# Kernel tuning notes

Hardware: AMD Instinct MI355X
Metric: run time of the kernel (lower is better)

Reference implementation:

```python
import jax, jax.numpy as jnp
import numpy as np

B, S, DIM, H, HD = 4, 1024, 1280, 16, 80
SCALE = HD ** -0.5
ROPE_THETA = 10000.0


def rotate_half(x):
    x1, x2 = jnp.split(x, 2, axis=-1)
    return jnp.concatenate([-x2, x1], axis=-1)


def setup_inputs() -> dict:
    key = jax.random.key(0)
    ks = jax.random.split(key, 5)
    x = jax.random.normal(ks[0], (B, S, DIM), dtype=jnp.float32)
    Wqkv = jax.random.normal(ks[1], (DIM, 3 * DIM), dtype=jnp.float32) * 0.02
    bqkv = jax.random.normal(ks[2], (3 * DIM,), dtype=jnp.float32) * 0.01
    Wproj = jax.random.normal(ks[3], (DIM, DIM), dtype=jnp.float32) * 0.02
    bproj = jax.random.normal(ks[4], (DIM,), dtype=jnp.float32) * 0.01
    # realistic rotary tables: (S, HD) with duplicated freq halves (matches rotate_half layout)
    inv_freq = 1.0 / (ROPE_THETA ** (jnp.arange(0, HD, 2, dtype=jnp.float32) / HD))
    freqs = jnp.outer(jnp.arange(S, dtype=jnp.float32), inv_freq)  # (S, HD/2)
    emb = jnp.concatenate([freqs, freqs], axis=-1)  # (S, HD)
    rope_cos = jnp.cos(emb)
    rope_sin = jnp.sin(emb)
    return {"x": x, "rope_cos": rope_cos, "rope_sin": rope_sin,
            "Wqkv": Wqkv, "bqkv": bqkv, "Wproj": Wproj, "bproj": bproj}


def reference(x, rope_cos, rope_sin, Wqkv, bqkv, Wproj, bproj):
    b, s, d = x.shape
    qkv = (x @ Wqkv + bqkv).reshape(b, s, 3, H, HD)
    q, k, v = qkv[:, :, 0], qkv[:, :, 1], qkv[:, :, 2]  # each (b, s, H, HD)
    cos = rope_cos[None, :, None, :]  # (1, s, 1, HD)
    sin = rope_sin[None, :, None, :]
    q = q * cos + rotate_half(q) * sin
    k = k * cos + rotate_half(k) * sin
    # SDPA with all-ones mask (full attention)
    scores = jnp.einsum("bqhd,bkhd->bhqk", q, k) * SCALE
    probs = jax.nn.softmax(scores, axis=-1)
    out = jnp.einsum("bhqk,bkhd->bqhd", probs, v).reshape(b, s, d)
    return out @ Wproj + bproj
```

## Files before the change

### kernel.cpp

```cpp
#include <hip/hip_runtime.h>
#include <math.h>

#define SCALE_F 0.11180339887498949f
#define HDP 96

typedef short  short8  __attribute__((ext_vector_type(8)));
typedef short  short4v __attribute__((ext_vector_type(4)));
typedef float  f32x4   __attribute__((ext_vector_type(4)));
typedef __bf16 bf16x8  __attribute__((ext_vector_type(8)));

__device__ __forceinline__ float bf2f(short s) {
  union { unsigned u; float f; } v;
  v.u = ((unsigned)(unsigned short)s) << 16;
  return v.f;
}
__device__ __forceinline__ short f2b(float f) {
  __bf16 h = (__bf16)f;
  return __builtin_bit_cast(short, h);
}
__device__ __forceinline__ bool probe_is_bf16(const unsigned* probe) {
  return (probe[1] & 0xFFFFu) != 0u;
}
__device__ __forceinline__ float load_scalar(const void* p, int i, bool isb) {
  return isb ? bf2f(((const short*)p)[i]) : ((const float*)p)[i];
}

__device__ __forceinline__ void gload_lds16(const short* g, short* l) {
  __builtin_amdgcn_global_load_lds(
      (const __attribute__((address_space(1))) void*)g,
      (__attribute__((address_space(3))) void*)l, 16, 0, 0);
}

template <typename V>
__device__ __forceinline__ auto mfma_try(V a, V b, f32x4 c, int)
    -> decltype(__builtin_amdgcn_mfma_f32_16x16x32_bf16(a, b, c, 0, 0, 0)) {
  return __builtin_amdgcn_mfma_f32_16x16x32_bf16(a, b, c, 0, 0, 0);
}
template <typename V>
__device__ __forceinline__ f32x4 mfma_try(V a, V b, f32x4 c, long) {
  return __builtin_amdgcn_mfma_f32_16x16x32_bf16(
      __builtin_bit_cast(bf16x8, a), __builtin_bit_cast(bf16x8, b), c, 0, 0, 0);
}
__device__ __forceinline__ f32x4 MFMA(short8 a, short8 b, f32x4 c) {
  return mfma_try(a, b, c, 0);
}

__global__ __launch_bounds__(256) void cvt_x_kernel(
    const void* __restrict__ xin, short* __restrict__ xout,
    const unsigned* __restrict__ probe) {
  bool isb = probe_is_bf16(probe);
  size_t i = ((size_t)blockIdx.x * 256 + threadIdx.x) * 8;
  if (isb) {
    *(short8*)&xout[i] = *(const short8*)((const short*)xin + i);
  } else {
    const float* f = (const float*)xin + i;
    float4 a0 = *(const float4*)f;
    float4 a1 = *(const float4*)(f + 4);
    short8 sv;
    sv[0] = f2b(a0.x); sv[1] = f2b(a0.y); sv[2] = f2b(a0.z); sv[3] = f2b(a0.w);
    sv[4] = f2b(a1.x); sv[5] = f2b(a1.y); sv[6] = f2b(a1.z); sv[7] = f2b(a1.w);
    *(short8*)&xout[i] = sv;
  }
}

__global__ __launch_bounds__(256) void transpose_kernel(
    const void* __restrict__ in, short* __restrict__ out, int R, int C,
    const unsigned* __restrict__ probe) {
  bool isb = probe_is_bf16(probe);
  __shared__ float tile[32][33];
  int t = threadIdx.x;
  int bx = blockIdx.x;
  int by = blockIdx.y;
  int r = t >> 3, c4 = (t & 7) * 4;
  size_t idx = (size_t)(by * 32 + r) * C + bx * 32 + c4;
  if (isb) {
    short4v v = *(const short4v*)((const short*)in + idx);
    tile[r][c4 + 0] = bf2f(v[0]);
    tile[r][c4 + 1] = bf2f(v[1]);
    tile[r][c4 + 2] = bf2f(v[2]);
    tile[r][c4 + 3] = bf2f(v[3]);
  } else {
    float4 v = *(const float4*)((const float*)in + idx);
    tile[r][c4 + 0] = v.x;
    tile[r][c4 + 1] = v.y;
    tile[r][c4 + 2] = v.z;
    tile[r][c4 + 3] = v.w;
  }
  __syncthreads();
  int rr = t >> 3, k4 = (t & 7) * 4;
  short4v o;
  o[0] = f2b(tile[k4 + 0][rr]);
  o[1] = f2b(tile[k4 + 1][rr]);
  o[2] = f2b(tile[k4 + 2][rr]);
  o[3] = f2b(tile[k4 + 3][rr]);
  *(short4v*)&out[(size_t)(bx * 32 + rr) * R + by * 32 + k4] = o;
}

__global__ __launch_bounds__(512, 2) void gemm_qkv_kernel(
    const short* __restrict__ X, const short* __restrict__ Wt,
    const void* __restrict__ bias, const unsigned* __restrict__ probe,
    short* __restrict__ Qw, short* __restrict__ Kw, short* __restrict__ Vt) {
  const int K = 1280;
  __shared__ short Al[2][2][8192];
  __shared__ short Bl[2][2][8192];
  int t = threadIdx.x;
  int bm = blockIdx.x / 15, bn = blockIdx.x % 15;
  int m0 = bm * 256, n0 = bn * 256;
  int w = t >> 6, lane = t & 63;
  int quad = lane >> 4, l16 = lane & 15, l8 = l16 & 7;
  int arow = (w >> 2) * 64 + l16;
  int brow = (w & 3) * 32 + l16;
  int sr = t >> 3, t8s = t * 8;
  int sjs = (t & 7) ^ (sr & 7);
  int soff0 = ((quad ^ l8) * 8);
  int soff1 = (((4 + quad) ^ l8) * 8);
  f32x4 acc[2][2][4][2] = {};
  short8 afr[4][2];
  short8 bf0[2][2], bf1[2][2];

#define STAGE8(PTR, R0, KOFF, LP)                                            \
  {                                                                          \
    const short* g_ = (PTR) + (size_t)((R0) + sr) * 1280 + (KOFF) + sjs * 8; \
    gload_lds16(g_, (LP) + t8s);                                             \
    gload_lds16(g_ + 64 * 1280, (LP) + t8s + 4096);                          \
  }

#define READ_A(S, H)                                                         \
  {                                                                          \
    _Pragma("unroll") for (int mt = 0; mt < 4; mt++) {                       \
      int rp_ = (arow + mt * 16) * 64;                                       \
      afr[mt][0] = *(const short8*)&Al[S][H][rp_ + soff0];                   \
      afr[mt][1] = *(const short8*)&Al[S][H][rp_ + soff1];                   \
    }                                                                        \
  }
#define READ_B(DST, S, H)                                                    \
  {                                                                          \
    _Pragma("unroll") for (int nt = 0; nt < 2; nt++) {                       \
      int rp_ = (brow + nt * 16) * 64;                                       \
      DST[nt][0] = *(const short8*)&Bl[S][H][rp_ + soff0];                   \
      DST[nt][1] = *(const short8*)&Bl[S][H][rp_ + soff1];                   \
    }                                                                        \
  }
#define MFMA16(QM, QN, BF, WAITI)                                            \
  {                                                                          \
    asm volatile("s_waitcnt lgkmcnt(" #WAITI ")" ::: "memory");              \
    __builtin_amdgcn_sched_barrier(0);                                       \
    __builtin_amdgcn_s_setprio(1);                                           \
    _Pragma("unroll") for (int mt = 0; mt < 4; mt++)                         \
      _Pragma("unroll") for (int nt = 0; nt < 2; nt++) {                     \
        acc[QM][QN][mt][nt] = MFMA(afr[mt][0], BF[nt][0], acc[QM][QN][mt][nt]); \
        acc[QM][QN][mt][nt] = MFMA(afr[mt][1], BF[nt][1], acc[QM][QN][mt][nt]); \
      }                                                                      \
    __builtin_amdgcn_s_setprio(0);                                           \
  }
#define BAR() __builtin_amdgcn_s_barrier()
#define VW4()                                                                \
  {                                                                          \
    asm volatile("s_waitcnt vmcnt(4)" ::: "memory");                         \
    __builtin_amdgcn_sched_barrier(0);                                       \
  }

  STAGE8(X,  m0,       0,  &Al[0][0][0]);
  STAGE8(X,  m0 + 128, 0,  &Al[0][1][0]);
  STAGE8(Wt, n0,       0,  &Bl[0][0][0]);
  STAGE8(Wt, n0 + 128, 0,  &Bl[0][1][0]);
  STAGE8(X,  m0,       64, &Al[1][0][0]);
  STAGE8(Wt, n0,       64, &Bl[1][0][0]);
  VW4();
  BAR();

  for (int i = 0; i < 10; i++) {
    int k1 = (2 * i + 1) * 64;
    int k2 = (2 * i + 2) * 64; if (k2 >= K) k2 = 0;
    int k3 = (2 * i + 3) * 64; if (k3 >= K) k3 = 0;
    READ_A(0, 0); READ_B(bf0, 0, 0); READ_B(bf1, 0, 1);
    STAGE8(X,  m0 + 128, k1, &Al[1][1][0]);
    MFMA16(0, 0, bf0, 4);
    BAR();
    STAGE8(Wt, n0 + 128, k1, &Bl[1][1][0]);
    MFMA16(0, 1, bf1, 0);
    BAR();
    READ_A(0, 1);
    STAGE8(X,  m0,       k2, &Al[0][0][0]);
    MFMA16(1, 0, bf0, 0);
    BAR();
    STAGE8(Wt, n0,       k2, &Bl[0][0][0]);
    MFMA16(1, 1, bf1, 0);
    VW4();
    BAR();
    READ_A(1, 0); READ_B(bf0, 1, 0); READ_B(bf1, 1, 1);
    STAGE8(X,  m0 + 128, k2, &Al[0][1][0]);
    MFMA16(0, 0, bf0, 4);
    BAR();
    STAGE8(Wt, n0 + 128, k2, &Bl[0][1][0]);
    MFMA16(0, 1, bf1, 0);
    BAR();
    READ_A(1, 1);
    STAGE8(X,  m0,       k3, &Al[1][0][0]);
    MFMA16(1, 0, bf0, 0);
    BAR();
    STAGE8(Wt, n0,       k3, &Bl[1][0][0]);
    MFMA16(1, 1, bf1, 0);
    VW4();
    BAR();
  }
  asm volatile("s_waitcnt vmcnt(0)" ::: "memory");
  __builtin_amdgcn_sched_barrier(0);

  bool isb = probe_is_bf16(probe);
  float bv[2][2];
#pragma unroll
  for (int qn = 0; qn < 2; qn++)
#pragma unroll
    for (int nt = 0; nt < 2; nt++)
      bv[qn][nt] =
          load_scalar(bias, n0 + qn * 128 + (w & 3) * 32 + nt * 16 + l16, isb);
#pragma unroll
  for (int qm = 0; qm < 2; qm++)
#pragma unroll
    for (int mt = 0; mt < 4; mt++) {
      int mbase = m0 + qm * 128 + (w >> 2) * 64 + mt * 16 + quad * 4;
      int b = mbase >> 10, sbase = mbase & 1023;
#pragma unroll
      for (int qn = 0; qn < 2; qn++)
#pragma unroll
        for (int nt = 0; nt < 2; nt++) {
          int n = n0 + qn * 128 + (w & 3) * 32 + nt * 16 + l16;
          int which = n / 1280;
          int rmod = n - which * 1280;
          int h = rmod / 80;
          int d = rmod - h * 80;
          int bh = b * 16 + h;
          if (which == 2) {
            short4v vv;
#pragma unroll
            for (int reg = 0; reg < 4; reg++)
              vv[reg] = f2b(acc[qm][qn][mt][nt][reg] + bv[qn][nt]);
            *(short4v*)&Vt[((size_t)bh * 80 + d) * 1024 + sbase] = vv;
          } else {
            short* dst = (which == 0 ? Qw : Kw);
#pragma unroll
            for (int reg = 0; reg < 4; reg++)
              dst[((size_t)bh * 1024 + sbase + reg) * HDP + d] =
                  f2b(acc[qm][qn][mt][nt][reg] + bv[qn][nt]);
          }
        }
    }
#undef STAGE8
#undef READ_A
#undef READ_B
#undef MFMA16
#undef BAR
#undef VW4
}

__global__ __launch_bounds__(256) void rope_kernel(
    short* __restrict__ Qw, short* __restrict__ Kw,
    const void* __restrict__ cosb, const void* __restrict__ sinb,
    const unsigned* __restrict__ probe) {
  bool isb = probe_is_bf16(probe);
  int t = threadIdx.x;
  int w = t >> 6, lane = t & 63;
  int job = blockIdx.x * 4 + w;
  int which = job & 1;
  int row = job >> 1;
  int s = row & 1023;
  short* ptr = (which ? Kw : Qw) + (size_t)row * HDP;
  float scale = which ? 1.0f : SCALE_F;
  if (lane < 40) {
    float p0 = bf2f(ptr[lane]);
    float p1 = bf2f(ptr[lane + 40]);
    float c0 = load_scalar(cosb, s * 80 + lane, isb);
    float s0 = load_scalar(sinb, s * 80 + lane, isb);
    float c1 = load_scalar(cosb, s * 80 + lane + 40, isb);
    float s1 = load_scalar(sinb, s * 80 + lane + 40, isb);
    ptr[lane] = f2b((p0 * c0 - p1 * s0) * scale);
    ptr[lane + 40] = f2b((p1 * c1 + p0 * s1) * scale);
  } else if (lane < 56) {
    ptr[40 + lane] = 0;
  }
}

__global__ __launch_bounds__(512, 4) void attn_kernel(
    const short* __restrict__ Qw, const short* __restrict__ Kw,
    const short* __restrict__ Vt, short* __restrict__ out) {
  __shared__ short Klds[2][64 * 104];
  __shared__ short Vlds[2][80 * 72];
  __shared__ short Ps[8][16 * 72];
  int t = threadIdx.x;
  int w = t >> 6, lane = t & 63;
  int quad = lane >> 4, l16 = lane & 15;
  int bh = blockIdx.x & 63;
  int qt = blockIdx.x >> 6;
  int q0 = qt * 128;
  const short* Kb = Kw + (size_t)bh * 1024 * HDP;
  const short* Vb = Vt + (size_t)bh * 80 * 1024;

  short8 aq[3];
  {
    const short* qrow = Qw + ((size_t)bh * 1024 + q0 + w * 16 + l16) * HDP;
#pragma unroll
    for (int ks = 0; ks < 3; ks++)
      aq[ks] = *(const short8*)&qrow[ks * 32 + quad * 8];
  }

  short8 kreg[2], vreg[2];
#define PREFETCH(c)                                                        \
  {                                                                        \
    {                                                                      \
      int row = t / 12, col = (t % 12) * 8;                                \
      kreg[0] = *(const short8*)&Kb[(size_t)((c) + row) * HDP + col];      \
    }                                                                      \
    if (t < 256) {                                                         \
      int idx = 512 + t;                                                   \
      int row = idx / 12, col = (idx % 12) * 8;                            \
      kreg[1] = *(const short8*)&Kb[(size_t)((c) + row) * HDP + col];      \
    }                                                                      \
    {                                                                      \
      int d = t >> 3, s0 = (t & 7) * 8;                                    \
      vreg[0] = *(const short8*)&Vb[(size_t)d * 1024 + (c) + s0];          \
    }                                                                      \
    if (t < 128) {                                                         \
      int idx = 512 + t;                                                   \
      int d = idx >> 3, s0 = (idx & 7) * 8;                                \
      vreg[1] = *(const short8*)&Vb[(size_t)d * 1024 + (c) + s0];          \
    }                                                                      \
  }
#define STORE_LDS(P)                                                       \
  {                                                                        \
    {                                                                      \
      int row = t / 12, col = (t % 12) * 8;                                \
      *(short8*)&Klds[P][row * 104 + col] = kreg[0];                       \
    }                                                                      \
    if (t < 256) {                                                         \
      int idx = 512 + t;                                                   \
      int row = idx / 12, col = (idx % 12) * 8;                            \
      *(short8*)&Klds[P][row * 104 + col] = kreg[1];                       \
    }                                                                      \
    {                                                                      \
      int d = t >> 3, s0 = (t & 7) * 8;                                    \
      *(short8*)&Vlds[P][d * 72 + s0] = vreg[0];                           \
    }                                                                      \
    if (t < 128) {                                                         \
      int idx = 512 + t;                                                   \
      int d = idx >> 3, s0 = (idx & 7) * 8;                                \
      *(short8*)&Vlds[P][d * 72 + s0] = vreg[1];                           \
    }                                                                      \
  }

  PREFETCH(0);
  STORE_LDS(0);
  __syncthreads();

  f32x4 ofr[5] = {};
  float lsum[4] = {0.f, 0.f, 0.f, 0.f};
  short* Pw = &Ps[w][0];

  int p = 0;
  for (int c = 0; c < 1024; c += 64, p ^= 1) {
    if (c + 64 < 1024) PREFETCH(c + 64);
    const short* Kl = &Klds[p][0];
    const short* Vl = &Vlds[p][0];
    f32x4 sf[4] = {};
#pragma unroll
    for (int nt = 0; nt < 4; nt++) {
      short8 bk0 = *(const short8*)&Kl[(nt * 16 + l16) * 104 + 0 * 32 + quad * 8];
      short8 bk1 = *(const short8*)&Kl[(nt * 16 + l16) * 104 + 1 * 32 + quad * 8];
      short8 bk2 = *(const short8*)&Kl[(nt * 16 + l16) * 104 + 2 * 32 + quad * 8];
      sf[nt] = MFMA(aq[0], bk0, sf[nt]);
      sf[nt] = MFMA(aq[1], bk1, sf[nt]);
      sf[nt] = MFMA(aq[2], bk2, sf[nt]);
    }
#pragma unroll
    for (int r = 0; r < 4; r++) {
      float p0 = __expf(fminf(sf[0][r], 30.f));
      float p1 = __expf(fminf(sf[1][r], 30.f));
      float p2 = __expf(fminf(sf[2][r], 30.f));
      float p3 = __expf(fminf(sf[3][r], 30.f));
      sf[0][r] = p0; sf[1][r] = p1; sf[2][r] = p2; sf[3][r] = p3;
      lsum[r] += (p0 + p1) + (p2 + p3);
    }
#pragma unroll
    for (int nt = 0; nt < 4; nt++)
#pragma unroll
      for (int r = 0; r < 4; r++)
        Pw[(quad * 4 + r) * 72 + nt * 16 + l16] = f2b(sf[nt][r]);
    __threadfence_block();
    short8 ap[2];
#pragma unroll
    for (int ks = 0; ks < 2; ks++)
      ap[ks] = *(const short8*)&Pw[l16 * 72 + ks * 32 + quad * 8];
#pragma unroll
    for (int nt = 0; nt < 5; nt++) {
      short8 bv0 = *(const short8*)&Vl[(nt * 16 + l16) * 72 + 0 * 32 + quad * 8];
      short8 bv1 = *(const short8*)&Vl[(nt * 16 + l16) * 72 + 1 * 32 + quad * 8];
      ofr[nt] = MFMA(ap[0], bv0, ofr[nt]);
      ofr[nt] = MFMA(ap[1], bv1, ofr[nt]);
    }
    if (c + 64 < 1024) {
      STORE_LDS(p ^ 1);
      __syncthreads();
    }
  }
#pragma unroll
  for (int off = 1; off < 16; off <<= 1)
#pragma unroll
    for (int r = 0; r < 4; r++) lsum[r] += __shfl_xor(lsum[r], off);
  float inv[4];
#pragma unroll
  for (int r = 0; r < 4; r++) inv[r] = 1.f / lsum[r];
  int b = bh >> 4, h = bh & 15;
#pragma unroll
  for (int nt = 0; nt < 5; nt++) {
    int d = nt * 16 + l16;
#pragma unroll
    for (int r = 0; r < 4; r++) {
      int s = q0 + w * 16 + quad * 4 + r;
      out[((size_t)(b * 1024 + s)) * 1280 + h * 80 + d] = f2b(ofr[nt][r] * inv[r]);
    }
  }
}

__global__ __launch_bounds__(256) void gemm_proj_kernel(
    const short* __restrict__ A, const short* __restrict__ Wt,
    const void* __restrict__ bias, const unsigned* __restrict__ probe,
    float* __restrict__ out) {
  const int K = 1280;
  __shared__ short As[2][128 * 32];
  __shared__ short Bs[2][128 * 32];
  int t = threadIdx.x;
  int bm = blockIdx.x / 10;
  int bn = blockIdx.x % 10;
  int m0 = bm * 128, n0 = bn * 128;
  int w = t >> 6, lane = t & 63;
  int wm = w & 1, wn = w >> 1;
  int quad = lane >> 4, l16 = lane & 15;
  int row = t >> 2, ch = (t & 3) * 8, row2 = row + 64;
  int t8 = t * 8;
  const short* Ar  = A  + (size_t)(m0 + row)  * K + ch;
  const short* Ar2 = A  + (size_t)(m0 + row2) * K + ch;
  const short* Wr  = Wt + (size_t)(n0 + row)  * K + ch;
  const short* Wr2 = Wt + (size_t)(n0 + row2) * K + ch;
  f32x4 acc[4][4] = {};
  gload_lds16(Ar,  &As[0][t8]);
  gload_lds16(Ar2, &As[0][t8 + 2048]);
  gload_lds16(Wr,  &Bs[0][t8]);
  gload_lds16(Wr2, &Bs[0][t8 + 2048]);
  __syncthreads();
  int p = 0;
#define PROJ_COMPUTE(pp)                                                      \
  {                                                                           \
    short8 af[4], bfr[4];                                                     \
    _Pragma("unroll") for (int mt = 0; mt < 4; mt++)                          \
        af[mt] = *(const short8*)&As[pp][(wm * 64 + mt * 16 + l16) * 32 + quad * 8]; \
    _Pragma("unroll") for (int nt = 0; nt < 4; nt++)                          \
        bfr[nt] = *(const short8*)&Bs[pp][(wn * 64 + nt * 16 + l16) * 32 + quad * 8]; \
    _Pragma("unroll") for (int mt = 0; mt < 4; mt++)                          \
        _Pragma("unroll") for (int nt = 0; nt < 4; nt++)                      \
            acc[mt][nt] = MFMA(af[mt], bfr[nt], acc[mt][nt]);                 \
  }
  for (int k0 = 32; k0 < K; k0 += 32, p ^= 1) {
    gload_lds16(Ar + k0,  &As[p ^ 1][t8]);
    gload_lds16(Ar2 + k0, &As[p ^ 1][t8 + 2048]);
    gload_lds16(Wr + k0,  &Bs[p ^ 1][t8]);
    gload_lds16(Wr2 + k0, &Bs[p ^ 1][t8 + 2048]);
    PROJ_COMPUTE(p);
    __syncthreads();
  }
  PROJ_COMPUTE(p);
  bool isb = probe_is_bf16(probe);
  float bv[4];
#pragma unroll
  for (int nt = 0; nt < 4; nt++)
    bv[nt] = load_scalar(bias, n0 + wn * 64 + nt * 16 + l16, isb);
#pragma unroll
  for (int mt = 0; mt < 4; mt++) {
#pragma unroll
    for (int nt = 0; nt < 4; nt++) {
      int n = n0 + wn * 64 + nt * 16 + l16;
#pragma unroll
      for (int reg = 0; reg < 4; reg++) {
        int m = m0 + wm * 64 + mt * 16 + quad * 4 + reg;
        out[(size_t)m * 1280 + n] = acc[mt][nt][reg] + bv[nt];
      }
    }
  }
}

extern "C" void kernel_launch(void* const* d_in, const int* in_sizes, int n_in,
                              void* d_out, int out_size, void* d_ws, size_t ws_size,
                              hipStream_t stream) {
  const void* x        = d_in[0];
  const void* rope_cos = d_in[1];
  const void* rope_sin = d_in[2];
  const void* Wqkv     = d_in[3];
  const void* bqkv     = d_in[4];
  const void* Wproj    = d_in[5];
  const void* bproj    = d_in[6];
  const unsigned* probe = (const unsigned*)rope_cos;
  char* ws = (char*)d_ws;
  short* Wt1 = (short*)(ws + 0);
  short* Wt2 = (short*)(ws + 9830400);
  short* Qw  = (short*)(ws + 13107200);
  short* Kw  = (short*)(ws + 25690112);
  short* Vt  = (short*)(ws + 38273024);
  short* Xb  = (short*)(ws + 48758784);
  short* At  = (short*)(ws + 48758784);

  cvt_x_kernel<<<2560, 256, 0, stream>>>(x, Xb, probe);
  transpose_kernel<<<dim3(3840 / 32, 1280 / 32), 256, 0, stream>>>(Wqkv, Wt1, 1280, 3840, probe);
  transpose_kernel<<<dim3(1280 / 32, 1280 / 32), 256, 0, stream>>>(Wproj, Wt2, 1280, 1280, probe);
  gemm_qkv_kernel<<<240, 512, 0, stream>>>(Xb, Wt1, bqkv, probe, Qw, Kw, Vt);
  rope_kernel<<<32768, 256, 0, stream>>>(Qw, Kw, rope_cos, rope_sin, probe);
  attn_kernel<<<512, 512, 0, stream>>>(Qw, Kw, Vt, At);
  gemm_proj_kernel<<<32 * 10, 256, 0, stream>>>(At, Wt2, bproj, probe, (float*)d_out);
}
```

Measured before the change: 244.2 us.

## Keep attention probabilities in registers by computing transposed scores

Swaps the QK^T MFMA operands so each lane holds scores for one query row, letting the exponentiated probabilities feed directly as the B operand of 16x16x16 bf16 MFMAs for the PV product. This removes the per-wave LDS staging buffer for P, its write/read round trip, and the fence, and it simplifies the row-sum reduction and the output stores into vectorized short4 writes. The trade-off is twice as many smaller-K MFMA instructions for PV and 8-byte V reads from LDS.

New measurement: 236.9 us. -3.0%, faster.

```diff
diff --git a/kernel.cpp b/kernel.cpp
--- a/kernel.cpp
+++ b/kernel.cpp
@@ -8,6 +8,7 @@
 typedef short  short4v __attribute__((ext_vector_type(4)));
 typedef float  f32x4   __attribute__((ext_vector_type(4)));
 typedef __bf16 bf16x8  __attribute__((ext_vector_type(8)));
+typedef __bf16 bf16x4  __attribute__((ext_vector_type(4)));
 
 __device__ __forceinline__ float bf2f(short s) {
   union { unsigned u; float f; } v;
@@ -44,6 +45,42 @@
 __device__ __forceinline__ f32x4 MFMA(short8 a, short8 b, f32x4 c) {
   return mfma_try(a, b, c, 0);
 }
+
+#if __has_builtin(__builtin_amdgcn_mfma_f32_16x16x16bf16_1k)
+template <typename V>
+__device__ __forceinline__ auto mfma16_try(V a, V b, f32x4 c, int)
+    -> decltype(__builtin_amdgcn_mfma_f32_16x16x16bf16_1k(a, b, c, 0, 0, 0)) {
+  return __builtin_amdgcn_mfma_f32_16x16x16bf16_1k(a, b, c, 0, 0, 0);
+}
+template <typename V>
+__device__ __forceinline__ f32x4 mfma16_try(V a, V b, f32x4 c, long) {
+  return __builtin_amdgcn_mfma_f32_16x16x16bf16_1k(
+      __builtin_bit_cast(bf16x4, a), __builtin_bit_cast(bf16x4, b), c, 0, 0, 0);
+}
+__device__ __forceinline__ f32x4 MFMA16(short4v a, short4v b, f32x4 c) {
+  return mfma16_try(a, b, c, 0);
+}
+#elif __has_builtin(__builtin_amdgcn_mfma_f32_16x16x16_bf16)
+template <typename V>
+__device__ __forceinline__ auto mfma16_try(V a, V b, f32x4 c, int)
+    -> decltype(__builtin_amdgcn_mfma_f32_16x16x16_bf16(a, b, c, 0, 0, 0)) {
+  return __builtin_amdgcn_mfma_f32_16x16x16_bf16(a, b, c, 0, 0, 0);
+}
+template <typename V>
+__device__ __forceinline__ f32x4 mfma16_try(V a, V b, f32x4 c, long) {
+  return __builtin_amdgcn_mfma_f32_16x16x16_bf16(
+      __builtin_bit_cast(bf16x4, a), __builtin_bit_cast(bf16x4, b), c, 0, 0, 0);
+}
+__device__ __forceinline__ f32x4 MFMA16(short4v a, short4v b, f32x4 c) {
+  return mfma16_try(a, b, c, 0);
+}
+#else
+__device__ __forceinline__ f32x4 MFMA16(short4v a, short4v b, f32x4 c) {
+  asm volatile("v_mfma_f32_16x16x16_bf16 %0, %1, %2, %0"
+               : "+v"(c) : "v"(a), "v"(b));
+  return c;
+}
+#endif
 
 __global__ __launch_bounds__(256) void cvt_x_kernel(
     const void* __restrict__ xin, short* __restrict__ xout,
@@ -141,7 +178,7 @@
       DST[nt][1] = *(const short8*)&Bl[S][H][rp_ + soff1];                   \
     }                                                                        \
   }
-#define MFMA16(QM, QN, BF, WAITI)                                            \
+#define MFMA16C(QM, QN, BF, WAITI)                                           \
   {                                                                          \
     asm volatile("s_waitcnt lgkmcnt(" #WAITI ")" ::: "memory");              \
     __builtin_amdgcn_sched_barrier(0);                                       \
@@ -175,32 +212,32 @@
     int k3 = (2 * i + 3) * 64; if (k3 >= K) k3 = 0;
     READ_A(0, 0); READ_B(bf0, 0, 0); READ_B(bf1, 0, 1);
     STAGE8(X,  m0 + 128, k1, &Al[1][1][0]);
-    MFMA16(0, 0, bf0, 4);
+    MFMA16C(0, 0, bf0, 4);
     BAR();
     STAGE8(Wt, n0 + 128, k1, &Bl[1][1][0]);
-    MFMA16(0, 1, bf1, 0);
+    MFMA16C(0, 1, bf1, 0);
     BAR();
     READ_A(0, 1);
     STAGE8(X,  m0,       k2, &Al[0][0][0]);
-    MFMA16(1, 0, bf0, 0);
+    MFMA16C(1, 0, bf0, 0);
     BAR();
     STAGE8(Wt, n0,       k2, &Bl[0][0][0]);
-    MFMA16(1, 1, bf1, 0);
+    MFMA16C(1, 1, bf1, 0);
     VW4();
     BAR();
     READ_A(1, 0); READ_B(bf0, 1, 0); READ_B(bf1, 1, 1);
     STAGE8(X,  m0 + 128, k2, &Al[0][1][0]);
-    MFMA16(0, 0, bf0, 4);
+    MFMA16C(0, 0, bf0, 4);
     BAR();
     STAGE8(Wt, n0 + 128, k2, &Bl[0][1][0]);
-    MFMA16(0, 1, bf1, 0);
+    MFMA16C(0, 1, bf1, 0);
     BAR();
     READ_A(1, 1);
     STAGE8(X,  m0,       k3, &Al[1][0][0]);
-    MFMA16(1, 0, bf0, 0);
+    MFMA16C(1, 0, bf0, 0);
     BAR();
     STAGE8(Wt, n0,       k3, &Bl[1][0][0]);
-    MFMA16(1, 1, bf1, 0);
+    MFMA16C(1, 1, bf1, 0);
     VW4();
     BAR();
   }
@@ -249,7 +286,7 @@
 #undef STAGE8
 #undef READ_A
 #undef READ_B
-#undef MFMA16
+#undef MFMA16C
 #undef BAR
 #undef VW4
 }
@@ -286,7 +323,6 @@
     const short* __restrict__ Vt, short* __restrict__ out) {
   __shared__ short Klds[2][64 * 104];
   __shared__ short Vlds[2][80 * 72];
-  __shared__ short Ps[8][16 * 72];
   int t = threadIdx.x;
   int w = t >> 6, lane = t & 63;
   int quad = lane >> 4, l16 = lane & 15;
@@ -353,8 +389,7 @@
   __syncthreads();
 
   f32x4 ofr[5] = {};
-  float lsum[4] = {0.f, 0.f, 0.f, 0.f};
-  short* Pw = &Ps[w][0];
+  float lsum = 0.f;
 
   int p = 0;
   for (int c = 0; c < 1024; c += 64, p ^= 1) {
@@ -367,57 +402,46 @@
       short8 bk0 = *(const short8*)&Kl[(nt * 16 + l16) * 104 + 0 * 32 + quad * 8];
       short8 bk1 = *(const short8*)&Kl[(nt * 16 + l16) * 104 + 1 * 32 + quad * 8];
       short8 bk2 = *(const short8*)&Kl[(nt * 16 + l16) * 104 + 2 * 32 + quad * 8];
-      sf[nt] = MFMA(aq[0], bk0, sf[nt]);
-      sf[nt] = MFMA(aq[1], bk1, sf[nt]);
-      sf[nt] = MFMA(aq[2], bk2, sf[nt]);
+      sf[nt] = MFMA(bk0, aq[0], sf[nt]);
+      sf[nt] = MFMA(bk1, aq[1], sf[nt]);
+      sf[nt] = MFMA(bk2, aq[2], sf[nt]);
     }
-#pragma unroll
-    for (int r = 0; r < 4; r++) {
-      float p0 = __expf(fminf(sf[0][r], 30.f));
-      float p1 = __expf(fminf(sf[1][r], 30.f));
-      float p2 = __expf(fminf(sf[2][r], 30.f));
-      float p3 = __expf(fminf(sf[3][r], 30.f));
-      sf[0][r] = p0; sf[1][r] = p1; sf[2][r] = p2; sf[3][r] = p3;
-      lsum[r] += (p0 + p1) + (p2 + p3);
+    short4v bp[4];
+#pragma unroll
+    for (int nt = 0; nt < 4; nt++) {
+      float e0 = __expf(fminf(sf[nt][0], 30.f));
+      float e1 = __expf(fminf(sf[nt][1], 30.f));
+      float e2 = __expf(fminf(sf[nt][2], 30.f));
+      float e3 = __expf(fminf(sf[nt][3], 30.f));
+      lsum += (e0 + e1) + (e2 + e3);
+      bp[nt][0] = f2b(e0); bp[nt][1] = f2b(e1);
+      bp[nt][2] = f2b(e2); bp[nt][3] = f2b(e3);
     }
 #pragma unroll
-    for (int nt = 0; nt < 4; nt++)
-#pragma unroll
-      for (int r = 0; r < 4; r++)
-        Pw[(quad * 4 + r) * 72 + nt * 16 + l16] = f2b(sf[nt][r]);
-    __threadfence_block();
-    short8 ap[2];
-#pragma unroll
-    for (int ks = 0; ks < 2; ks++)
-      ap[ks] = *(const short8*)&Pw[l16 * 72 + ks * 32 + quad * 8];
-#pragma unroll
-    for (int nt = 0; nt < 5; nt++) {
-      short8 bv0 = *(const short8*)&Vl[(nt * 16 + l16) * 72 + 0 * 32 + quad * 8];
-      short8 bv1 = *(const short8*)&Vl[(nt * 16 + l16) * 72 + 1 * 32 + quad * 8];
-      ofr[nt] = MFMA(ap[0], bv0, ofr[nt]);
-      ofr[nt] = MFMA(ap[1], bv1, ofr[nt]);
-    }
+    for (int cc = 0; cc < 4; cc++)
+#pragma unroll
+      for (int nt5 = 0; nt5 < 5; nt5++) {
+        short4v va =
+            *(const short4v*)&Vl[(nt5 * 16 + l16) * 72 + cc * 16 + quad * 4];
+        ofr[nt5] = MFMA16(va, bp[cc], ofr[nt5]);
+      }
     if (c + 64 < 1024) {
       STORE_LDS(p ^ 1);
       __syncthreads();
     }
   }
-#pragma unroll
-  for (int off = 1; off < 16; off <<= 1)
-#pragma unroll
-    for (int r = 0; r < 4; r++) lsum[r] += __shfl_xor(lsum[r], off);
-  float inv[4];
-#pragma unroll
-  for (int r = 0; r < 4; r++) inv[r] = 1.f / lsum[r];
+  lsum += __shfl_xor(lsum, 16);
+  lsum += __shfl_xor(lsum, 32);
+  float inv = 1.f / lsum;
   int b = bh >> 4, h = bh & 15;
-#pragma unroll
-  for (int nt = 0; nt < 5; nt++) {
-    int d = nt * 16 + l16;
-#pragma unroll
-    for (int r = 0; r < 4; r++) {
-      int s = q0 + w * 16 + quad * 4 + r;
-      out[((size_t)(b * 1024 + s)) * 1280 + h * 80 + d] = f2b(ofr[nt][r] * inv[r]);
-    }
+  int s = q0 + w * 16 + l16;
+#pragma unroll
+  for (int nt5 = 0; nt5 < 5; nt5++) {
+    short4v o;
+#pragma unroll
+    for (int j = 0; j < 4; j++) o[j] = f2b(ofr[nt5][j] * inv);
+    *(short4v*)&out[((size_t)(b * 1024 + s)) * 1280 + h * 80 + nt5 * 16 +
+                    quad * 4] = o;
   }
 }
 
```
